# Optimization experiments

Hardware: AMD Instinct MI355X
Metric: run time of the kernel (lower is better)

## Reference

```python
import jax, jax.numpy as jnp
import numpy as np

# Episode structure: C classes, NS support + NQ query samples per class, D-dim embeddings, S sectors.
C, NS, NQ, D, S = 2048, 5, 25, 64, 32
PER = NS + NQ  # samples per class (contiguous block layout)


def _pairwise_dist(a, b):
    # Euclidean distance matrix [len(a), len(b)] without materializing [Qa, Qb, D] diffs.
    d2 = (a * a).sum(-1)[:, None] + (b * b).sum(-1)[None, :] - 2.0 * (a @ b.T)
    return jnp.sqrt(jnp.clip(d2, 0.0))


def setup_inputs() -> dict:
    key = jax.random.key(0)
    x = jax.random.normal(key, (C * PER, D), dtype=jnp.float32)
    # episodic layout: class c occupies rows [c*PER, (c+1)*PER); first NS are support
    target = jnp.repeat(jnp.arange(C, dtype=jnp.int32), PER)
    class_sector = jnp.arange(C, dtype=jnp.int32) % S  # class_to_sector routing table
    return {"input": x, "target": target, "class_sector": class_sector}


def reference(input, target, class_sector):
    x3 = input.reshape(C, PER, D)
    # class prototypes = mean of support embeddings
    protos = x3[:, :NS].mean(axis=1)                      # [C, D]
    queries = x3[:, NS:].reshape(C * NQ, D)               # [Q, D]
    true_cls = target.reshape(C, PER)[:, NS:].reshape(-1)  # [Q]

    # sector prototypes = mean of class prototypes per sector
    counts = jax.ops.segment_sum(jnp.ones((C,), input.dtype), class_sector, num_segments=S)
    sec_protos = jax.ops.segment_sum(protos, class_sector, num_segments=S) / counts[:, None]  # [S, D]

    # hierarchical routing: nearest sector per query, then argmin over classes in that sector
    sec = jnp.argmin(_pairwise_dist(queries, sec_protos), axis=1)  # [Q]
    dqc = _pairwise_dist(queries, protos)                          # [Q, C] (dominant intermediate)
    in_sector = class_sector[None, :] == sec[:, None]              # [Q, C]
    pred = jnp.argmin(jnp.where(in_sector, dqc, jnp.inf), axis=1)  # predicted class id

    # loss uses FULL distance logits (as in the original), predictions use the hierarchical route
    logp = jax.nn.log_softmax(-dqc, axis=1)
    loss = -jnp.take_along_axis(logp, true_cls[:, None].astype(jnp.int32), axis=1).mean()
    acc = (pred.astype(jnp.int32) == true_cls).astype(jnp.float32).mean()
    return loss, acc
```

## Files before the change

### kernel.cpp

```cpp
#include <hip/hip_runtime.h>
#include <hip/hip_bf16.h>

constexpr int kC   = 2048;
constexpr int kNS  = 5;
constexpr int kNQ  = 25;
constexpr int kPER = 30;
constexpr int kD   = 64;
constexpr int kS   = 32;
constexpr int kQ   = kC * kNQ;
constexpr int kSplit = 8;
constexpr int kSubt  = (kC / kSplit) / 16;
constexpr int kCPS   = kC / kSplit;
constexpr int kTPS   = kQ / 32;
constexpr int kFinBlocks = kQ / 256;

constexpr float kLOG2E = 1.44269504088896340736f;
constexpr float kC2    = kLOG2E * kLOG2E;
constexpr float kNEG2C = -2.0f * kC2;
constexpr float kBIG   = 1e30f;

constexpr size_t OP_PROT = 0;
constexpr size_t OP_PSWZ = OP_PROT + (size_t)kC * kD;
constexpr size_t OP_PN   = OP_PSWZ + (size_t)kC * kD / 2;
constexpr size_t OP_PNC2 = OP_PN + kC;
constexpr size_t OP_SSWH = OP_PNC2 + kC;
constexpr size_t OP_SSWL = OP_SSWH + (size_t)kS * kD / 2;
constexpr size_t OP_SN   = OP_SSWL + (size_t)kS * kD / 2;
constexpr size_t OP_QNC  = OP_SN + kS;
constexpr size_t OP_QSEC = OP_QNC + kQ;
constexpr size_t OP_DT   = OP_QSEC + kQ;
constexpr size_t OP_TC   = OP_DT + kQ;
constexpr size_t OP_S2   = OP_TC + kQ;
constexpr size_t OP_PB   = OP_S2 + (size_t)kSplit * kQ;
constexpr size_t OP_ACC  = OP_PB + (size_t)kSplit * kQ;
constexpr size_t OP_TICK = OP_ACC + 2;

typedef __attribute__((ext_vector_type(8))) short short8;
typedef __attribute__((ext_vector_type(4))) float f32x4;

__device__ inline ushort f2bf(float f) {
    __hip_bfloat16 h = __float2bfloat16(f);
    return *reinterpret_cast<ushort*>(&h);
}
__device__ inline float bf2f(ushort u) {
    uint v = ((uint)u) << 16;
    return __int_as_float((int)v);
}
__device__ inline short8 pack_hi(float4 a, float4 b) {
    short8 r;
    r[0] = (short)f2bf(a.x); r[1] = (short)f2bf(a.y);
    r[2] = (short)f2bf(a.z); r[3] = (short)f2bf(a.w);
    r[4] = (short)f2bf(b.x); r[5] = (short)f2bf(b.y);
    r[6] = (short)f2bf(b.z); r[7] = (short)f2bf(b.w);
    return r;
}
__device__ inline void packhl(float4 a, float4 b, short8& hi, short8& lo) {
    float v[8] = {a.x, a.y, a.z, a.w, b.x, b.y, b.z, b.w};
#pragma unroll
    for (int i = 0; i < 8; ++i) {
        ushort h = f2bf(v[i]);
        hi[i] = (short)h;
        lo[i] = (short)f2bf(v[i] - bf2f(h));
    }
}

__global__ void k_prep(const float* __restrict__ x, float* __restrict__ ws) {
    int c = blockIdx.x, d = threadIdx.x;
    const float* base = x + (size_t)c * kPER * kD + d;
    float p = 0.f;
#pragma unroll
    for (int s = 0; s < kNS; ++s) p += base[s * kD];
    p *= (1.f / kNS);
    ws[OP_PROT + (size_t)c * kD + d] = p;
    ((ushort*)(ws + OP_PSWZ))[((c >> 4) * 1024) + ((d >> 3) * 128) + ((c & 15) * 8) + (d & 7)] = f2bf(p);
    float sq = p * p;
    for (int off = 32; off; off >>= 1) sq += __shfl_down(sq, off);
    if (d == 0) {
        ws[OP_PN + c] = sq;
        ws[OP_PNC2 + c] = sq * kC2;
    }
    if (c == 0 && d == 0) {
        ws[OP_ACC] = 0.f;
        ws[OP_ACC + 1] = 0.f;
        ((int*)ws)[OP_TICK] = 0;
    }
}

__global__ __launch_bounds__(256) void k_sec(const int* __restrict__ csec,
                                             float* __restrict__ ws) {
    __shared__ float sAcc[4][kD];
    int s = blockIdx.x;
    int w = threadIdx.x >> 6, d = threadIdx.x & 63;
    float acc = 0.f;
#pragma unroll
    for (int j = 0; j < 16; ++j) {
        int c = s + 32 * (w + 4 * j);
        acc += ws[OP_PROT + (size_t)c * kD + d];
    }
    sAcc[w][d] = acc;
    __syncthreads();
    if (w == 0) {
        float sp = (sAcc[0][d] + sAcc[1][d] + sAcc[2][d] + sAcc[3][d]) * (1.f / 64.f);
        ushort h = f2bf(sp);
        ushort l = f2bf(sp - bf2f(h));
        int idx = ((s >> 4) * 1024) + ((d >> 3) * 128) + ((s & 15) * 8) + (d & 7);
        ((ushort*)(ws + OP_SSWH))[idx] = h;
        ((ushort*)(ws + OP_SSWL))[idx] = l;
        float sq = sp * sp;
        for (int off = 32; off; off >>= 1) sq += __shfl_down(sq, off);
        if (d == 0) ws[OP_SN + s] = sq;
    }
}

__global__ __launch_bounds__(256) void k_qprep(const float* __restrict__ x,
                                               const int* __restrict__ target,
                                               float* __restrict__ ws) {
    int t = threadIdx.x;
    int w = t >> 6, lane = t & 63;
    int lrow = lane & 15, lgr = lane >> 4;
    int qt = blockIdx.x * 4 + w;
    int q = qt * 16 + lrow;
    int row = (q / kNQ) * kPER + kNS + q % kNQ;
    const float* qr = x + (size_t)row * kD + lgr * 8;
    float4 qa0 = *(const float4*)qr,        qa1 = *(const float4*)(qr + 4);
    float4 qb0 = *(const float4*)(qr + 32), qb1 = *(const float4*)(qr + 36);

    float qn = qa0.x*qa0.x + qa0.y*qa0.y + qa0.z*qa0.z + qa0.w*qa0.w
             + qa1.x*qa1.x + qa1.y*qa1.y + qa1.z*qa1.z + qa1.w*qa1.w
             + qb0.x*qb0.x + qb0.y*qb0.y + qb0.z*qb0.z + qb0.w*qb0.w
             + qb1.x*qb1.x + qb1.y*qb1.y + qb1.z*qb1.z + qb1.w*qb1.w;
    qn += __shfl_xor(qn, 16);
    qn += __shfl_xor(qn, 32);

    int tc = target[row];
    const float* pr = ws + OP_PROT + (size_t)tc * kD + lgr * 8;
    float4 p00 = *(const float4*)pr,        p01 = *(const float4*)(pr + 4);
    float4 p10 = *(const float4*)(pr + 32), p11 = *(const float4*)(pr + 36);
    float dot = qa0.x*p00.x + qa0.y*p00.y + qa0.z*p00.z + qa0.w*p00.w
              + qa1.x*p01.x + qa1.y*p01.y + qa1.z*p01.z + qa1.w*p01.w
              + qb0.x*p10.x + qb0.y*p10.y + qb0.z*p10.z + qb0.w*p10.w
              + qb1.x*p11.x + qb1.y*p11.y + qb1.z*p11.z + qb1.w*p11.w;
    dot += __shfl_xor(dot, 16);
    dot += __shfl_xor(dot, 32);
    float dtrue = sqrtf(fmaxf(qn + ws[OP_PN + tc] - 2.f * dot, 0.f));

    short8 b0h, b0l, b1h, b1l;
    packhl(qa0, qa1, b0h, b0l);
    packhl(qb0, qb1, b1h, b1l);

    const ushort* ssh = (const ushort*)(ws + OP_SSWH);
    const ushort* ssl = (const ushort*)(ws + OP_SSWL);
    float bestS = INFINITY;
    int qsec = 0;
#pragma unroll
    for (int st = 0; st < 2; ++st) {
        short8 sh0 = *(const short8*)(ssh + st * 1024 + lane * 8);
        short8 sh1 = *(const short8*)(ssh + st * 1024 + 512 + lane * 8);
        short8 sl0 = *(const short8*)(ssl + st * 1024 + lane * 8);
        short8 sl1 = *(const short8*)(ssl + st * 1024 + 512 + lane * 8);
        f32x4 dh = {0.f, 0.f, 0.f, 0.f};
        dh = __builtin_amdgcn_mfma_f32_16x16x32_bf16(sh0, b0h, dh, 0, 0, 0);
        dh = __builtin_amdgcn_mfma_f32_16x16x32_bf16(sh1, b1h, dh, 0, 0, 0);
        dh = __builtin_amdgcn_mfma_f32_16x16x32_bf16(sh0, b0l, dh, 0, 0, 0);
        dh = __builtin_amdgcn_mfma_f32_16x16x32_bf16(sh1, b1l, dh, 0, 0, 0);
        dh = __builtin_amdgcn_mfma_f32_16x16x32_bf16(sl0, b0h, dh, 0, 0, 0);
        dh = __builtin_amdgcn_mfma_f32_16x16x32_bf16(sl1, b1h, dh, 0, 0, 0);
        f32x4 sn4 = *(const f32x4*)(ws + OP_SN + st * 16 + lgr * 4);
#pragma unroll
        for (int r2 = 0; r2 < 4; ++r2) {
            float score = fmaf(dh[r2], -2.f, sn4[r2]);
            int idx = st * 16 + lgr * 4 + r2;
            if (score < bestS) { bestS = score; qsec = idx; }
        }
    }
#pragma unroll
    for (int off = 16; off <= 32; off <<= 1) {
        float ob = __shfl_xor(bestS, off);
        int oi = __shfl_xor(qsec, off);
        if (ob < bestS || (ob == bestS && oi < qsec)) { bestS = ob; qsec = oi; }
    }
    if (lane < 16) {
        ws[OP_QNC + q] = qn * kC2;
        ((int*)ws)[OP_QSEC + q] = qsec;
        ws[OP_DT + q] = dtrue;
        ((int*)ws)[OP_TC + q] = tc;
    }
}

__global__ __launch_bounds__(256) void k_main(const float* __restrict__ x,
                                              float* __restrict__ ws) {
    __shared__ ushort sP[kSubt * 1024 + 1024];
    __shared__ float sPn[kSubt * 16 + 16];

    int t = threadIdx.x;
    int w = t >> 6, lane = t & 63;
    int lrow = lane & 15, lgr = lane >> 4;
    int task = blockIdx.x * 4 + w;
    int split = task / kTPS;
    int qt = task - split * kTPS;
    int qbase = qt * 32;
    int q1 = qbase + lrow, q2 = qbase + 16 + lrow;

    {
        const float4* gsrc = (const float4*)((const ushort*)(ws + OP_PSWZ) + (size_t)split * kSubt * 1024);
        float4* ldst = (float4*)sP;
#pragma unroll
        for (int j = 0; j < 8; ++j) ldst[t + j * 256] = gsrc[t + j * 256];
        sPn[t] = ws[OP_PNC2 + split * kCPS + t];
    }

    int row1 = (q1 / kNQ) * kPER + kNS + q1 % kNQ;
    int row2 = (q2 / kNQ) * kPER + kNS + q2 % kNQ;
    const float* qr1 = x + (size_t)row1 * kD + lgr * 8;
    const float* qr2 = x + (size_t)row2 * kD + lgr * 8;
    float4 a10 = *(const float4*)qr1,        a11 = *(const float4*)(qr1 + 4);
    float4 a12 = *(const float4*)(qr1 + 32), a13 = *(const float4*)(qr1 + 36);
    float4 a20 = *(const float4*)qr2,        a21 = *(const float4*)(qr2 + 4);
    float4 a22 = *(const float4*)(qr2 + 32), a23 = *(const float4*)(qr2 + 36);
    short8 b0h1 = pack_hi(a10, a11), b1h1 = pack_hi(a12, a13);
    short8 b0h2 = pack_hi(a20, a21), b1h2 = pack_hi(a22, a23);

    float qn1 = ws[OP_QNC + q1];
    float qn2 = ws[OP_QNC + q2];
    int qsec1 = ((const int*)ws)[OP_QSEC + q1];
    int qsec2 = ((const int*)ws)[OP_QSEC + q2];

    bool m1a = (qsec1 & 1), m1b = (qsec1 >> 1) & 1, p1 = (qsec1 >> 4) & 1;
    float actb1 = (((qsec1 & 15) >> 2) == lgr) ? 0.f : kBIG;
    bool m2a = (qsec2 & 1), m2b = (qsec2 >> 1) & 1, p2 = (qsec2 >> 4) & 1;
    float actb2 = (((qsec2 & 15) >> 2) == lgr) ? 0.f : kBIG;

    float S0 = 0.f, S1 = 0.f, S2 = 0.f, S3 = 0.f;
    float S4 = 0.f, S5 = 0.f, S6 = 0.f, S7 = 0.f;
    uint Kk1 = ~0u, Kk2 = ~0u;

    __syncthreads();

    int lofs = lane * 8;
    const ushort* lp = sP + lofs;
    const float* lpn = sPn + lgr * 4;
    short8 pa0 = *(const short8*)lp;
    short8 pa1 = *(const short8*)(lp + 512);
    f32x4 pnC = *(const f32x4*)lpn;

#define SM(D, ACCR, PQ, S)                                                 \
    float D = fmaf(ACCR, kNEG2C, PQ);                                      \
    S += __builtin_amdgcn_exp2f(-__builtin_amdgcn_sqrtf(D));

#define AMIN(E0, E1, E2, E3, O0, O1, O2, O3, MA, MB, P, ACTB, K)           \
    {                                                                      \
        float s01 = MA ? E1 : E0;                                          \
        float s23 = MA ? E3 : E2;                                          \
        float sE = MB ? s23 : s01;                                         \
        float t01 = MA ? O1 : O0;                                          \
        float t23 = MA ? O3 : O2;                                          \
        float sO = MB ? t23 : t01;                                         \
        float sel = (P ? sO : sE) + ACTB;                                  \
        uint key = (__float_as_uint(sel) & 0xFFFFFFF8u) | it;              \
        K = key < K ? key : K;                                             \
    }

    for (uint it = 0; it < (uint)(kSubt / 2); ++it) {
        f32x4 aE1 = {0.f, 0.f, 0.f, 0.f}, aE2 = {0.f, 0.f, 0.f, 0.f};
        aE1 = __builtin_amdgcn_mfma_f32_16x16x32_bf16(pa0, b0h1, aE1, 0, 0, 0);
        aE1 = __builtin_amdgcn_mfma_f32_16x16x32_bf16(pa1, b1h1, aE1, 0, 0, 0);
        aE2 = __builtin_amdgcn_mfma_f32_16x16x32_bf16(pa0, b0h2, aE2, 0, 0, 0);
        aE2 = __builtin_amdgcn_mfma_f32_16x16x32_bf16(pa1, b1h2, aE2, 0, 0, 0);
        f32x4 pnE = pnC;
        lp += 1024; lpn += 16;
        pa0 = *(const short8*)lp;
        pa1 = *(const short8*)(lp + 512);
        pnC = *(const f32x4*)lpn;

        float pqE10 = pnE[0] + qn1, pqE11 = pnE[1] + qn1;
        float pqE12 = pnE[2] + qn1, pqE13 = pnE[3] + qn1;
        float pqE20 = pnE[0] + qn2, pqE21 = pnE[1] + qn2;
        float pqE22 = pnE[2] + qn2, pqE23 = pnE[3] + qn2;
        SM(e10, aE1[0], pqE10, S0)
        SM(e11, aE1[1], pqE11, S1)
        SM(e12, aE1[2], pqE12, S2)
        SM(e13, aE1[3], pqE13, S3)
        SM(e20, aE2[0], pqE20, S4)
        SM(e21, aE2[1], pqE21, S5)
        SM(e22, aE2[2], pqE22, S6)
        SM(e23, aE2[3], pqE23, S7)

        f32x4 aO1 = {0.f, 0.f, 0.f, 0.f}, aO2 = {0.f, 0.f, 0.f, 0.f};
        aO1 = __builtin_amdgcn_mfma_f32_16x16x32_bf16(pa0, b0h1, aO1, 0, 0, 0);
        aO1 = __builtin_amdgcn_mfma_f32_16x16x32_bf16(pa1, b1h1, aO1, 0, 0, 0);
        aO2 = __builtin_amdgcn_mfma_f32_16x16x32_bf16(pa0, b0h2, aO2, 0, 0, 0);
        aO2 = __builtin_amdgcn_mfma_f32_16x16x32_bf16(pa1, b1h2, aO2, 0, 0, 0);
        f32x4 pnO = pnC;
        lp += 1024; lpn += 16;
        pa0 = *(const short8*)lp;
        pa1 = *(const short8*)(lp + 512);
        pnC = *(const f32x4*)lpn;

        float pqO10 = pnO[0] + qn1, pqO11 = pnO[1] + qn1;
        float pqO12 = pnO[2] + qn1, pqO13 = pnO[3] + qn1;
        float pqO20 = pnO[0] + qn2, pqO21 = pnO[1] + qn2;
        float pqO22 = pnO[2] + qn2, pqO23 = pnO[3] + qn2;
        SM(o10, aO1[0], pqO10, S0)
        SM(o11, aO1[1], pqO11, S1)
        SM(o12, aO1[2], pqO12, S2)
        SM(o13, aO1[3], pqO13, S3)
        SM(o20, aO2[0], pqO20, S4)
        SM(o21, aO2[1], pqO21, S5)
        SM(o22, aO2[2], pqO22, S6)
        SM(o23, aO2[3], pqO23, S7)

        AMIN(e10, e11, e12, e13, o10, o11, o12, o13, m1a, m1b, p1, actb1, Kk1)
        AMIN(e20, e21, e22, e23, o20, o21, o22, o23, m2a, m2b, p2, actb2, Kk2)
    }
#undef SM
#undef AMIN

    float Ss1 = (S0 + S1) + (S2 + S3);
    float Ss2 = (S4 + S5) + (S6 + S7);
#pragma unroll
    for (int off = 16; off <= 32; off <<= 1) {
        Ss1 += __shfl_xor(Ss1, off);
        uint ok = __shfl_xor(Kk1, off);
        Kk1 = ok < Kk1 ? ok : Kk1;
        Ss2 += __shfl_xor(Ss2, off);
        uint ok2 = __shfl_xor(Kk2, off);
        Kk2 = ok2 < Kk2 ? ok2 : Kk2;
    }
    if (lane < 16) {
        size_t o1 = (size_t)split * kQ + q1;
        ws[OP_S2 + o1] = Ss1;
        ((uint*)ws)[OP_PB + o1] = Kk1;
        size_t o2 = (size_t)split * kQ + q2;
        ws[OP_S2 + o2] = Ss2;
        ((uint*)ws)[OP_PB + o2] = Kk2;
    }
}

__global__ __launch_bounds__(256) void k_fin(float* __restrict__ ws,
                                             float* __restrict__ out) {
    int t = threadIdx.x;
    int q = blockIdx.x * 256 + t;

    float S = 0.f;
    uint best = ~0u;
    int ksel = 0;
#pragma unroll
    for (int k = 0; k < kSplit; ++k) {
        size_t o = (size_t)k * kQ + q;
        S += ws[OP_S2 + o];
        uint kk = ((const uint*)ws)[OP_PB + o];
        if (kk < best) { best = kk; ksel = k; }
    }
    int qsec = ((const int*)ws)[OP_QSEC + q];
    int it = (int)(best & 7u);
    int besti = ksel * kCPS + (2 * it + ((qsec >> 4) & 1)) * 16
              + ((qsec & 15) >> 2) * 4 + (qsec & 3);

    float loss = ws[OP_DT + q] + logf(S);
    float corr = (besti == ((const int*)ws)[OP_TC + q]) ? 1.f : 0.f;

    __shared__ float rl[256], rc[256];
    rl[t] = loss;
    rc[t] = corr;
    __syncthreads();
    for (int off = 128; off; off >>= 1) {
        if (t < off) { rl[t] += rl[t + off]; rc[t] += rc[t + off]; }
        __syncthreads();
    }
    if (t == 0) {
        atomicAdd(ws + OP_ACC, rl[0]);
        atomicAdd(ws + OP_ACC + 1, rc[0]);
        __threadfence();
        int old = atomicAdd((int*)ws + OP_TICK, 1);
        if (old == kFinBlocks - 1) {
            __threadfence();
            float L = atomicAdd(ws + OP_ACC, 0.f);
            float A = atomicAdd(ws + OP_ACC + 1, 0.f);
            out[0] = L / (float)kQ;
            out[1] = A / (float)kQ;
        }
    }
}

extern "C" void kernel_launch(void* const* d_in, const int* in_sizes, int n_in,
                              void* d_out, int out_size, void* d_ws, size_t ws_size,
                              hipStream_t stream) {
    const float* x = (const float*)d_in[0];
    const int* target = (const int*)d_in[1];
    const int* csec = (const int*)d_in[2];
    float* out = (float*)d_out;
    float* ws = (float*)d_ws;

    k_prep<<<kC, kD, 0, stream>>>(x, ws);
    k_sec<<<kS, 256, 0, stream>>>(csec, ws);
    k_qprep<<<kQ / 16 / 4, 256, 0, stream>>>(x, target, ws);
    k_main<<<kTPS * kSplit / 4, 256, 0, stream>>>(x, ws);
    k_fin<<<kFinBlocks, 256, 0, stream>>>(ws, out);
}
```

Measured before the change: 63.78 us.

## Fold distance bias into MFMA accumulator and use 512-thread blocks per split

Prototypes are pre-scaled by -2·log2e² when converted to bf16, and the MFMA accumulator is seeded with pn+qn, so the distance comes straight out of the matrix unit with no per-element FMA. The main kernel also moves to 8 waves per block that share one split's prototype tile in LDS, which halves the number of tile loads per query. Scaling before bf16 rounding slightly changes precision. Larger blocks may reduce the number of resident blocks per CU.

After: 60.64 us. 4.9% less time.

```diff
diff --git a/kernel.cpp b/kernel.cpp
--- a/kernel.cpp
+++ b/kernel.cpp
@@ -12,6 +12,7 @@
 constexpr int kSubt  = (kC / kSplit) / 16;
 constexpr int kCPS   = kC / kSplit;
 constexpr int kTPS   = kQ / 32;
+constexpr int kBlkPerSplit = kTPS / 8;
 constexpr int kFinBlocks = kQ / 256;
 
 constexpr float kLOG2E = 1.44269504088896340736f;
@@ -72,7 +73,8 @@
     for (int s = 0; s < kNS; ++s) p += base[s * kD];
     p *= (1.f / kNS);
     ws[OP_PROT + (size_t)c * kD + d] = p;
-    ((ushort*)(ws + OP_PSWZ))[((c >> 4) * 1024) + ((d >> 3) * 128) + ((c & 15) * 8) + (d & 7)] = f2bf(p);
+    ((ushort*)(ws + OP_PSWZ))[((c >> 4) * 1024) + ((d >> 3) * 128) + ((c & 15) * 8) + (d & 7)] =
+        f2bf(p * kNEG2C);
     float sq = p * p;
     for (int off = 32; off; off >>= 1) sq += __shfl_down(sq, off);
     if (d == 0) {
@@ -187,7 +189,7 @@
     }
 }
 
-__global__ __launch_bounds__(256) void k_main(const float* __restrict__ x,
+__global__ __launch_bounds__(512) void k_main(const float* __restrict__ x,
                                               float* __restrict__ ws) {
     __shared__ ushort sP[kSubt * 1024 + 1024];
     __shared__ float sPn[kSubt * 16 + 16];
@@ -195,9 +197,8 @@
     int t = threadIdx.x;
     int w = t >> 6, lane = t & 63;
     int lrow = lane & 15, lgr = lane >> 4;
-    int task = blockIdx.x * 4 + w;
-    int split = task / kTPS;
-    int qt = task - split * kTPS;
+    int split = blockIdx.x / kBlkPerSplit;
+    int qt = (blockIdx.x % kBlkPerSplit) * 8 + w;
     int qbase = qt * 32;
     int q1 = qbase + lrow, q2 = qbase + 16 + lrow;
 
@@ -205,8 +206,8 @@
         const float4* gsrc = (const float4*)((const ushort*)(ws + OP_PSWZ) + (size_t)split * kSubt * 1024);
         float4* ldst = (float4*)sP;
 #pragma unroll
-        for (int j = 0; j < 8; ++j) ldst[t + j * 256] = gsrc[t + j * 256];
-        sPn[t] = ws[OP_PNC2 + split * kCPS + t];
+        for (int j = 0; j < 4; ++j) ldst[t + j * 512] = gsrc[t + j * 512];
+        if (t < kCPS) sPn[t] = ws[OP_PNC2 + split * kCPS + t];
     }
 
     int row1 = (q1 / kNQ) * kPER + kNS + q1 % kNQ;
@@ -243,9 +244,7 @@
     short8 pa1 = *(const short8*)(lp + 512);
     f32x4 pnC = *(const f32x4*)lpn;
 
-#define SM(D, ACCR, PQ, S)                                                 \
-    float D = fmaf(ACCR, kNEG2C, PQ);                                      \
-    S += __builtin_amdgcn_exp2f(-__builtin_amdgcn_sqrtf(D));
+#define SM(ACCR, S) S += __builtin_amdgcn_exp2f(-__builtin_amdgcn_sqrtf(ACCR));
 
 #define AMIN(E0, E1, E2, E3, O0, O1, O2, O3, MA, MB, P, ACTB, K)           \
     {                                                                      \
@@ -261,56 +260,38 @@
     }
 
     for (uint it = 0; it < (uint)(kSubt / 2); ++it) {
-        f32x4 aE1 = {0.f, 0.f, 0.f, 0.f}, aE2 = {0.f, 0.f, 0.f, 0.f};
-        aE1 = __builtin_amdgcn_mfma_f32_16x16x32_bf16(pa0, b0h1, aE1, 0, 0, 0);
+        f32x4 cE1 = pnC + qn1;
+        f32x4 cE2 = pnC + qn2;
+        f32x4 aE1 = __builtin_amdgcn_mfma_f32_16x16x32_bf16(pa0, b0h1, cE1, 0, 0, 0);
         aE1 = __builtin_amdgcn_mfma_f32_16x16x32_bf16(pa1, b1h1, aE1, 0, 0, 0);
-        aE2 = __builtin_amdgcn_mfma_f32_16x16x32_bf16(pa0, b0h2, aE2, 0, 0, 0);
+        f32x4 aE2 = __builtin_amdgcn_mfma_f32_16x16x32_bf16(pa0, b0h2, cE2, 0, 0, 0);
         aE2 = __builtin_amdgcn_mfma_f32_16x16x32_bf16(pa1, b1h2, aE2, 0, 0, 0);
-        f32x4 pnE = pnC;
         lp += 1024; lpn += 16;
         pa0 = *(const short8*)lp;
         pa1 = *(const short8*)(lp + 512);
         pnC = *(const f32x4*)lpn;
 
-        float pqE10 = pnE[0] + qn1, pqE11 = pnE[1] + qn1;
-        float pqE12 = pnE[2] + qn1, pqE13 = pnE[3] + qn1;
-        float pqE20 = pnE[0] + qn2, pqE21 = pnE[1] + qn2;
-        float pqE22 = pnE[2] + qn2, pqE23 = pnE[3] + qn2;
-        SM(e10, aE1[0], pqE10, S0)
-        SM(e11, aE1[1], pqE11, S1)
-        SM(e12, aE1[2], pqE12, S2)
-        SM(e13, aE1[3], pqE13, S3)
-        SM(e20, aE2[0], pqE20, S4)
-        SM(e21, aE2[1], pqE21, S5)
-        SM(e22, aE2[2], pqE22, S6)
-        SM(e23, aE2[3], pqE23, S7)
-
-        f32x4 aO1 = {0.f, 0.f, 0.f, 0.f}, aO2 = {0.f, 0.f, 0.f, 0.f};
-        aO1 = __builtin_amdgcn_mfma_f32_16x16x32_bf16(pa0, b0h1, aO1, 0, 0, 0);
+        SM(aE1[0], S0) SM(aE1[1], S1) SM(aE1[2], S2) SM(aE1[3], S3)
+        SM(aE2[0], S4) SM(aE2[1], S5) SM(aE2[2], S6) SM(aE2[3], S7)
+
+        f32x4 cO1 = pnC + qn1;
+        f32x4 cO2 = pnC + qn2;
+        f32x4 aO1 = __builtin_amdgcn_mfma_f32_16x16x32_bf16(pa0, b0h1, cO1, 0, 0, 0);
         aO1 = __builtin_amdgcn_mfma_f32_16x16x32_bf16(pa1, b1h1, aO1, 0, 0, 0);
-        aO2 = __builtin_amdgcn_mfma_f32_16x16x32_bf16(pa0, b0h2, aO2, 0, 0, 0);
+        f32x4 aO2 = __builtin_amdgcn_mfma_f32_16x16x32_bf16(pa0, b0h2, cO2, 0, 0, 0);
         aO2 = __builtin_amdgcn_mfma_f32_16x16x32_bf16(pa1, b1h2, aO2, 0, 0, 0);
-        f32x4 pnO = pnC;
         lp += 1024; lpn += 16;
         pa0 = *(const short8*)lp;
         pa1 = *(const short8*)(lp + 512);
         pnC = *(const f32x4*)lpn;
 
-        float pqO10 = pnO[0] + qn1, pqO11 = pnO[1] + qn1;
-        float pqO12 = pnO[2] + qn1, pqO13 = pnO[3] + qn1;
-        float pqO20 = pnO[0] + qn2, pqO21 = pnO[1] + qn2;
-        float pqO22 = pnO[2] + qn2, pqO23 = pnO[3] + qn2;
-        SM(o10, aO1[0], pqO10, S0)
-        SM(o11, aO1[1], pqO11, S1)
-        SM(o12, aO1[2], pqO12, S2)
-        SM(o13, aO1[3], pqO13, S3)
-        SM(o20, aO2[0], pqO20, S4)
-        SM(o21, aO2[1], pqO21, S5)
-        SM(o22, aO2[2], pqO22, S6)
-        SM(o23, aO2[3], pqO23, S7)
-
-        AMIN(e10, e11, e12, e13, o10, o11, o12, o13, m1a, m1b, p1, actb1, Kk1)
-        AMIN(e20, e21, e22, e23, o20, o21, o22, o23, m2a, m2b, p2, actb2, Kk2)
+        SM(aO1[0], S0) SM(aO1[1], S1) SM(aO1[2], S2) SM(aO1[3], S3)
+        SM(aO2[0], S4) SM(aO2[1], S5) SM(aO2[2], S6) SM(aO2[3], S7)
+
+        AMIN(aE1[0], aE1[1], aE1[2], aE1[3], aO1[0], aO1[1], aO1[2], aO1[3],
+             m1a, m1b, p1, actb1, Kk1)
+        AMIN(aE2[0], aE2[1], aE2[2], aE2[3], aO2[0], aO2[1], aO2[2], aO2[3],
+             m2a, m2b, p2, actb2, Kk2)
     }
 #undef SM
 #undef AMIN
@@ -394,6 +375,6 @@
     k_prep<<<kC, kD, 0, stream>>>(x, ws);
     k_sec<<<kS, 256, 0, stream>>>(csec, ws);
     k_qprep<<<kQ / 16 / 4, 256, 0, stream>>>(x, target, ws);
-    k_main<<<kTPS * kSplit / 4, 256, 0, stream>>>(x, ws);
+    k_main<<<kBlkPerSplit * kSplit, 512, 0, stream>>>(x, ws);
     k_fin<<<kFinBlocks, 256, 0, stream>>>(ws, out);
 }
```
